# Kernel tuning notes

Hardware: AMD Instinct MI355X
Metric: run time of the kernel (lower is better)

Reference implementation:

```python
import jax, jax.numpy as jnp
import numpy as np

B = 8192
IN = 2048   # input_size
H = 2048    # hidden_size
D = IN + H  # combine feature dim = 4096


def setup_inputs() -> dict:
    key = jax.random.key(0)
    ks = jax.random.split(key, 11)
    s = 1.0 / np.sqrt(D)  # nn.Linear default init scale
    inp = {
        "input": jax.random.normal(ks[0], (B, D), jnp.float32),
        "hidden": jax.random.normal(ks[1], (B, D), jnp.float32),
        "cell": jax.random.normal(ks[2], (B, H), jnp.float32),
        "Wf": jax.random.uniform(ks[3], (D, H), jnp.float32, -s, s),
        "bf": jax.random.uniform(ks[4], (H,), jnp.float32, -s, s),
        "Wc": jax.random.uniform(ks[5], (D, H), jnp.float32, -s, s),
        "bc": jax.random.uniform(ks[6], (H,), jnp.float32, -s, s),
        "Wi": jax.random.uniform(ks[7], (D, H), jnp.float32, -s, s),
        "bi": jax.random.uniform(ks[8], (H,), jnp.float32, -s, s),
        "Wo": jax.random.uniform(ks[9], (D, H), jnp.float32, -s, s),
        "bo": jax.random.uniform(ks[10], (H,), jnp.float32, -s, s),
    }
    return inp


def reference(input, hidden, cell, Wf, bf, Wc, bc, Wi, bi, Wo, bo):
    combine = input + hidden  # [B, D] elementwise add (as in source, not concat)
    # Fuse the 4 gate GEMMs into one [D, 4H] GEMM for efficiency (same math).
    W = jnp.concatenate([Wf, Wc, Wi, Wo], axis=1)  # [D, 4H]
    b = jnp.concatenate([bf, bc, bi, bo])          # [4H]
    gates = combine @ W + b                        # [B, 4H]
    gf, gc, gi, go = jnp.split(gates, 4, axis=1)
    ft = jax.nn.sigmoid(gf)
    ct_ = jnp.tanh(gc)
    it = jax.nn.sigmoid(jax.nn.sigmoid(gi))  # double sigmoid, faithful to source
    cell_state = cell * ft + ct_ * it
    out = jax.nn.sigmoid(go)
    hidden_state = out * jnp.tanh(cell_state)
    return (out, hidden_state, cell_state)
```

## Files before the change

### kernel.cpp

```cpp
#include <hip/hip_runtime.h>
#include <hip/hip_bf16.h>

#define B_SZ 8192
#define D_SZ 4096
#define H_SZ 2048
#define N4H  8192
#define NT   (D_SZ / 64)

typedef __attribute__((ext_vector_type(8))) __bf16 bf16x8;
typedef __attribute__((ext_vector_type(4))) float f32x4;

#define GPTR(p) ((__attribute__((address_space(1))) void*)(p))
#define LPTR(p) ((__attribute__((address_space(3))) void*)(p))

__global__ void prep_k(const float* __restrict__ x, const float* __restrict__ h,
                       __hip_bfloat16* __restrict__ comb,
                       const float* __restrict__ Wf, const float* __restrict__ Wc,
                       const float* __restrict__ Wi, const float* __restrict__ Wo,
                       __hip_bfloat16* __restrict__ WT) {
    __shared__ float t[32][33];
    if (blockIdx.x < 2048) {
        const size_t n4 = (size_t)B_SZ * D_SZ / 4;
        const size_t stride = (size_t)2048 * 256;
        for (size_t i = (size_t)blockIdx.x * 256 + threadIdx.x; i < n4; i += stride) {
            f32x4 a = __builtin_nontemporal_load((const f32x4*)x + i);
            f32x4 b = __builtin_nontemporal_load((const f32x4*)h + i);
            short4 r;
            r.x = __builtin_bit_cast(short, __float2bfloat16(a.x + b.x));
            r.y = __builtin_bit_cast(short, __float2bfloat16(a.y + b.y));
            r.z = __builtin_bit_cast(short, __float2bfloat16(a.z + b.z));
            r.w = __builtin_bit_cast(short, __float2bfloat16(a.w + b.w));
            ((short4*)comb)[i] = r;
        }
    } else {
        const int b = blockIdx.x - 2048;
        const int k0 = (b & 127) * 32;
        const int n0 = (b >> 7) * 32;
        const float* W = (n0 < H_SZ) ? Wf : (n0 < 2 * H_SZ) ? Wc
                       : (n0 < 3 * H_SZ) ? Wi : Wo;
        const int g = n0 >> 11;
        const int nc = n0 & (H_SZ - 1);
        const int tx = threadIdx.x & 31, ty = threadIdx.x >> 5;
#pragma unroll
        for (int j = 0; j < 4; ++j)
            t[ty + j * 8][tx] = __builtin_nontemporal_load(
                W + (size_t)(k0 + ty + j * 8) * H_SZ + nc + tx);
        __syncthreads();
#pragma unroll
        for (int j = 0; j < 4; ++j) {
            const int h2 = nc + ty + j * 8;
            const int np = ((h2 >> 4) << 6) + (g << 4) + (h2 & 15);
            WT[(size_t)np * D_SZ + k0 + tx] = __float2bfloat16(t[tx][ty + j * 8]);
        }
    }
}


#define LDS_A0 0
#define LDS_A1 16384
#define LDS_BB0 32768
#define LDS_BB1 49152

#define BAR()                                    \
    do {                                         \
        asm volatile("" ::: "memory");           \
        __builtin_amdgcn_s_barrier();            \
        asm volatile("" ::: "memory");           \
    } while (0)

#define STAGE_A(h, kt)                                                                 \
    do {                                                                               \
        _Pragma("unroll") for (int c_ = 0; c_ < 4; ++c_) {                             \
            __builtin_amdgcn_global_load_lds(                                          \
                GPTR(pA + (size_t)((c_ >> 1) * 128 + (h) * 64 + (c_ & 1) * 32) * D_SZ  \
                         + (size_t)(kt) * 64),                                         \
                LPTR(smem + (h) * 16384 + c_ * 4096 + wave * 1024), 16, 0, 0);         \
        }                                                                              \
    } while (0)

#define STAGE_B(qn, kt, bb)                                                            \
    do {                                                                               \
        _Pragma("unroll") for (int c_ = 0; c_ < 2; ++c_) {                             \
            __builtin_amdgcn_global_load_lds(                                          \
                GPTR(pB + (size_t)((qn) * 32 + c_ * 64) * D_SZ + (size_t)(kt) * 64),   \
                LPTR(smem + (bb) + (qn) * 8192 + c_ * 4096 + wave * 1024), 16, 0, 0);  \
        }                                                                              \
    } while (0)

#define LDA(dst, RB)                                                                   \
    do {                                                                               \
        _Pragma("unroll") for (int mi = 0; mi < 4; ++mi) {                             \
            const int row_ = wr * 64 + mi * 16 + fr;                                   \
            dst[mi][0] = *(const bf16x8*)(smem + (RB) + row_ * 128 + sw0);             \
            dst[mi][1] = *(const bf16x8*)(smem + (RB) + row_ * 128 + sw1);             \
        }                                                                              \
    } while (0)

#define LDB(dst, BB, qn)                                                               \
    do {                                                                               \
        _Pragma("unroll") for (int nf = 0; nf < 2; ++nf) {                             \
            const int row_ = (qn) * 64 + wc * 32 + nf * 16 + fr;                       \
            dst[nf][0] = *(const bf16x8*)(smem + (BB) + row_ * 128 + sw0);             \
            dst[nf][1] = *(const bf16x8*)(smem + (BB) + row_ * 128 + sw1);             \
        }                                                                              \
    } while (0)

#define MFMA_Q(qm, qn, areg, breg)                                                     \
    do {                                                                               \
        _Pragma("unroll") for (int mi = 0; mi < 4; ++mi)                               \
        _Pragma("unroll") for (int nf = 0; nf < 2; ++nf)                               \
        _Pragma("unroll") for (int ks = 0; ks < 2; ++ks)                               \
            acc[(qm) * 4 + mi][(qn) * 2 + nf] =                                        \
                __builtin_amdgcn_mfma_f32_16x16x32_bf16(                               \
                    areg[mi][ks], breg[nf][ks],                                        \
                    acc[(qm) * 4 + mi][(qn) * 2 + nf], 0, 0, 0);                       \
    } while (0)

#define TILE(KT, CURB, OTHB)                                                           \
    {                                                                                  \
        const int kt_ = (KT) & 63;                                                     \
                             \
        STAGE_B(0, kt_, OTHB);                                                         \
        LDA(a, LDS_A0);                                                                \
        LDB(b0, CURB, 0);                                                              \
        __builtin_amdgcn_s_setprio(1);                                                 \
        MFMA_Q(0, 0, a, b0);                                                           \
        __builtin_amdgcn_s_setprio(0);                                                 \
        asm volatile("s_waitcnt vmcnt(6)" ::: "memory");                               \
        BAR();                                                                         \
                     \
        STAGE_A(0, kt_);                                                               \
        LDB(b1, CURB, 1);                                                              \
        __builtin_amdgcn_s_setprio(1);                                                 \
        MFMA_Q(0, 1, a, b1);                                                           \
        __builtin_amdgcn_s_setprio(0);                                                 \
        asm volatile("s_waitcnt vmcnt(6)" ::: "memory");                               \
        BAR();                                                                         \
                  \
        STAGE_B(1, kt_, OTHB);                                                         \
        LDA(a, LDS_A1);                                                                \
        __builtin_amdgcn_s_setprio(1);                                                 \
        MFMA_Q(1, 0, a, b0);                                                           \
        __builtin_amdgcn_s_setprio(0);                                                 \
        BAR();                                                                         \
                                  \
        STAGE_A(1, kt_);                                                               \
        __builtin_amdgcn_s_setprio(1);                                                 \
        MFMA_Q(1, 1, a, b1);                                                           \
        __builtin_amdgcn_s_setprio(0);                                                 \
        asm volatile("s_waitcnt vmcnt(6)" ::: "memory");                               \
        BAR();                                                                         \
    }

__device__ __forceinline__ float fsig(float x) { return 1.f / (1.f + __expf(-x)); }
__device__ __forceinline__ float ftanh(float x) {
    x = fminf(fmaxf(x, -15.f), 15.f);
    float e = __expf(2.f * x);
    return (e - 1.f) / (e + 1.f);
}

__global__ __launch_bounds__(256, 2) void gemm4_k(
    const __hip_bfloat16* __restrict__ A,
    const __hip_bfloat16* __restrict__ BT,
    const float* __restrict__ cell,
    const float* __restrict__ bfb, const float* __restrict__ bcb,
    const float* __restrict__ bib, const float* __restrict__ bob,
    float* __restrict__ out)
{
    extern __shared__ char smem[];

    const int tid  = threadIdx.x;
    const int wave = tid >> 6;
    const int lane = tid & 63;
    const int wr = wave >> 1;
    const int wc = wave & 1;
    const int fr = lane & 15;
    const int sw0 = (((lane >> 4) + 0) ^ (fr & 7)) << 4;
    const int sw1 = (((lane >> 4) + 4) ^ (fr & 7)) << 4;

    const int wg = (blockIdx.x & 7) * 256 + (blockIdx.x >> 3);
    const int ntile = wg & 63;
    const int m0 = (wg >> 6) * 256;
    const int n0 = ntile * 128;

    const int r0   = tid >> 3;
    const int col0 = ((tid & 7) ^ (r0 & 7)) << 3;
    const __hip_bfloat16* pA = A  + (size_t)(m0 + r0) * D_SZ + col0;
    const __hip_bfloat16* pB = BT + (size_t)(n0 + r0) * D_SZ + col0;

    f32x4 acc[8][4] = {};
    bf16x8 a[4][2], b0[2][2], b1[2][2];

    STAGE_B(0, 0, LDS_BB0);
    STAGE_A(0, 0);
    STAGE_B(1, 0, LDS_BB0);
    STAGE_A(1, 0);
    asm volatile("s_waitcnt vmcnt(6)" ::: "memory");
    BAR();

#pragma unroll 1
    for (int t = 0; t < NT; t += 2) {
        TILE(t + 1, LDS_BB0, LDS_BB1);
        TILE(t + 2, LDS_BB1, LDS_BB0);
    }

    {
        const int crow = (lane >> 4) * 4;
        const int ccol = lane & 15;
        const int hh = (ntile * 2 + wc) * 16 + ccol;
        const float bf_ = bfb[hh], bc_ = bcb[hh], bi_ = bib[hh], bo_ = bob[hh];
        const size_t BH = (size_t)B_SZ * H_SZ;
        float* hidp = out + BH;
        float* cstp = out + 2 * BH;
#pragma unroll
        for (int ai = 0; ai < 8; ++ai) {
#pragma unroll
            for (int j = 0; j < 4; ++j) {
                const size_t r = (size_t)(m0 + wr * 128 + ai * 16 + crow + j);
                const size_t idx = r * H_SZ + hh;
                const float gf = acc[ai][0][j] + bf_;
                const float gc = acc[ai][1][j] + bc_;
                const float gi = acc[ai][2][j] + bi_;
                const float go = acc[ai][3][j] + bo_;
                const float ft = fsig(gf);
                const float ct = ftanh(gc);
                const float it_ = fsig(fsig(gi));
                const float ot = fsig(go);
                const float cv = __builtin_nontemporal_load(cell + idx);
                const float cs = cv * ft + ct * it_;
                __builtin_nontemporal_store(ot, out + idx);
                __builtin_nontemporal_store(cs, cstp + idx);
                __builtin_nontemporal_store(ot * ftanh(cs), hidp + idx);
            }
        }
    }

    asm volatile("s_waitcnt vmcnt(0)" ::: "memory");
}

extern "C" void kernel_launch(void* const* d_in, const int* in_sizes, int n_in,
                              void* d_out, int out_size, void* d_ws, size_t ws_size,
                              hipStream_t stream) {
    const float* input  = (const float*)d_in[0];
    const float* hidden = (const float*)d_in[1];
    const float* cell   = (const float*)d_in[2];
    const float* Wf     = (const float*)d_in[3];
    const float* bfb    = (const float*)d_in[4];
    const float* Wc     = (const float*)d_in[5];
    const float* bcb    = (const float*)d_in[6];
    const float* Wi     = (const float*)d_in[7];
    const float* bib    = (const float*)d_in[8];
    const float* Wo     = (const float*)d_in[9];
    const float* bob    = (const float*)d_in[10];
    float* out = (float*)d_out;

    char* ws = (char*)d_ws;
    __hip_bfloat16* comb = (__hip_bfloat16*)ws;
    __hip_bfloat16* WT   = (__hip_bfloat16*)(ws + (size_t)B_SZ * D_SZ * 2);

    hipFuncSetAttribute(reinterpret_cast<const void*>(gemm4_k),
                        hipFuncAttributeMaxDynamicSharedMemorySize, 65536);

    prep_k<<<2048 + 32768, 256, 0, stream>>>(input, hidden, comb, Wf, Wc, Wi, Wo, WT);
    gemm4_k<<<2048, 256, 65536, stream>>>(comb, WT, cell, bfb, bcb, bib, bob, out);
}
```

Before: 598.5 us.

## Switch fused-gate GEMM to 32x32x16 MFMA with 128x256 tiles

Replaces the 16x16x32 bf16 MFMA tiling with 32x32x16 MFMAs. The block tile changes from 256x128 to 128x256 and the weight interleave goes from 16-column to 32-column gate groups, so each wave still holds all four gates for its columns. Staging, LDS layout and the epilogue row mapping are reworked to match, and dynamic LDS grows to 80KB. The aim is fewer MFMA issues and LDS reads per FLOP, at the cost of more LDS per block, which may hurt occupancy at two blocks per CU.

```diff
diff --git a/kernel.cpp b/kernel.cpp
--- a/kernel.cpp
+++ b/kernel.cpp
@@ -7,8 +7,9 @@
 #define N4H  8192
 #define NT   (D_SZ / 64)
 
-typedef __attribute__((ext_vector_type(8))) __bf16 bf16x8;
-typedef __attribute__((ext_vector_type(4))) float f32x4;
+typedef __attribute__((ext_vector_type(8)))  __bf16 bf16x8;
+typedef __attribute__((ext_vector_type(4)))  float  f32x4;
+typedef __attribute__((ext_vector_type(16))) float  f32x16;
 
 #define GPTR(p) ((__attribute__((address_space(1))) void*)(p))
 #define LPTR(p) ((__attribute__((address_space(3))) void*)(p))
@@ -49,16 +50,14 @@
 #pragma unroll
         for (int j = 0; j < 4; ++j) {
             const int h2 = nc + ty + j * 8;
-            const int np = ((h2 >> 4) << 6) + (g << 4) + (h2 & 15);
+            const int np = ((h2 >> 5) << 7) + (g << 5) + (h2 & 31);
             WT[(size_t)np * D_SZ + k0 + tx] = __float2bfloat16(t[tx][ty + j * 8]);
         }
     }
 }
 
 
-#define LDS_A0 0
-#define LDS_A1 16384
-#define LDS_BB0 32768
+#define LDS_BB0 16384
 #define LDS_BB1 49152
 
 #define BAR()                                    \
@@ -68,85 +67,78 @@
         asm volatile("" ::: "memory");           \
     } while (0)
 
-#define STAGE_A(h, kt)                                                                 \
+#define STAGE_A(mt, kt)                                                                \
+    do {                                                                               \
+        _Pragma("unroll") for (int c_ = 0; c_ < 2; ++c_) {                             \
+            const int ro_ = c_ * 64 + (mt) * 32;                                       \
+            __builtin_amdgcn_global_load_lds(                                          \
+                GPTR(pA + (size_t)ro_ * D_SZ + (size_t)(kt) * 64),                     \
+                LPTR(smem + (ro_ + wave * 8) * 128), 16, 0, 0);                        \
+        }                                                                              \
+    } while (0)
+
+#define STAGE_Bp(jp, kt, bb)                                                           \
     do {                                                                               \
         _Pragma("unroll") for (int c_ = 0; c_ < 4; ++c_) {                             \
+            const int ro_ = (c_ >> 1) * 128 + (jp) * 64 + (c_ & 1) * 32;               \
             __builtin_amdgcn_global_load_lds(                                          \
-                GPTR(pA + (size_t)((c_ >> 1) * 128 + (h) * 64 + (c_ & 1) * 32) * D_SZ  \
-                         + (size_t)(kt) * 64),                                         \
-                LPTR(smem + (h) * 16384 + c_ * 4096 + wave * 1024), 16, 0, 0);         \
+                GPTR(pB + (size_t)ro_ * D_SZ + (size_t)(kt) * 64),                     \
+                LPTR(smem + (bb) + (ro_ + wave * 8) * 128), 16, 0, 0);                 \
         }                                                                              \
     } while (0)
 
-#define STAGE_B(qn, kt, bb)                                                            \
-    do {                                                                               \
-        _Pragma("unroll") for (int c_ = 0; c_ < 2; ++c_) {                             \
-            __builtin_amdgcn_global_load_lds(                                          \
-                GPTR(pB + (size_t)((qn) * 32 + c_ * 64) * D_SZ + (size_t)(kt) * 64),   \
-                LPTR(smem + (bb) + (qn) * 8192 + c_ * 4096 + wave * 1024), 16, 0, 0);  \
-        }                                                                              \
-    } while (0)
-
-#define LDA(dst, RB)                                                                   \
-    do {                                                                               \
-        _Pragma("unroll") for (int mi = 0; mi < 4; ++mi) {                             \
-            const int row_ = wr * 64 + mi * 16 + fr;                                   \
-            dst[mi][0] = *(const bf16x8*)(smem + (RB) + row_ * 128 + sw0);             \
-            dst[mi][1] = *(const bf16x8*)(smem + (RB) + row_ * 128 + sw1);             \
-        }                                                                              \
-    } while (0)
-
-#define LDB(dst, BB, qn)                                                               \
-    do {                                                                               \
-        _Pragma("unroll") for (int nf = 0; nf < 2; ++nf) {                             \
-            const int row_ = (qn) * 64 + wc * 32 + nf * 16 + fr;                       \
-            dst[nf][0] = *(const bf16x8*)(smem + (BB) + row_ * 128 + sw0);             \
-            dst[nf][1] = *(const bf16x8*)(smem + (BB) + row_ * 128 + sw1);             \
-        }                                                                              \
-    } while (0)
-
-#define MFMA_Q(qm, qn, areg, breg)                                                     \
-    do {                                                                               \
-        _Pragma("unroll") for (int mi = 0; mi < 4; ++mi)                               \
-        _Pragma("unroll") for (int nf = 0; nf < 2; ++nf)                               \
-        _Pragma("unroll") for (int ks = 0; ks < 2; ++ks)                               \
-            acc[(qm) * 4 + mi][(qn) * 2 + nf] =                                        \
-                __builtin_amdgcn_mfma_f32_16x16x32_bf16(                               \
-                    areg[mi][ks], breg[nf][ks],                                        \
-                    acc[(qm) * 4 + mi][(qn) * 2 + nf], 0, 0, 0);                       \
+#define LDA(mt, AOFF)                                                                  \
+    do {                                                                               \
+        _Pragma("unroll") for (int k_ = 0; k_ < 4; ++k_)                               \
+            a[mt][k_] = *(const bf16x8*)(smem + (AOFF) + swk[k_]);                     \
+    } while (0)
+
+#define LDB2(jp, BUFB)                                                                 \
+    do {                                                                               \
+        _Pragma("unroll") for (int jj_ = 0; jj_ < 2; ++jj_)                            \
+        _Pragma("unroll") for (int k_ = 0; k_ < 4; ++k_)                               \
+            b[jj_][k_] = *(const bf16x8*)(smem + (BUFB) + boff[(jp) * 2 + jj_]         \
+                                          + swk[k_]);                                  \
+    } while (0)
+
+#define MFMA_P(mt, jp)                                                                 \
+    do {                                                                               \
+        _Pragma("unroll") for (int k_ = 0; k_ < 4; ++k_)                               \
+        _Pragma("unroll") for (int jj_ = 0; jj_ < 2; ++jj_)                            \
+            acc[mt][(jp) * 2 + jj_] = __builtin_amdgcn_mfma_f32_32x32x16_bf16(         \
+                a[mt][k_], b[jj_][k_], acc[mt][(jp) * 2 + jj_], 0, 0, 0);              \
     } while (0)
 
 #define TILE(KT, CURB, OTHB)                                                           \
     {                                                                                  \
         const int kt_ = (KT) & 63;                                                     \
-                             \
-        STAGE_B(0, kt_, OTHB);                                                         \
-        LDA(a, LDS_A0);                                                                \
-        LDB(b0, CURB, 0);                                                              \
-        __builtin_amdgcn_s_setprio(1);                                                 \
-        MFMA_Q(0, 0, a, b0);                                                           \
-        __builtin_amdgcn_s_setprio(0);                                                 \
-        asm volatile("s_waitcnt vmcnt(6)" ::: "memory");                               \
-        BAR();                                                                         \
-                     \
+                                                                              \
+        STAGE_Bp(0, kt_, OTHB);                                                        \
+        LDA(0, aoff0);                                                                 \
+        LDB2(0, CURB);                                                                 \
+        __builtin_amdgcn_s_setprio(1);                                                 \
+        MFMA_P(0, 0);                                                                  \
+        __builtin_amdgcn_s_setprio(0);                                                 \
+        asm volatile("s_waitcnt vmcnt(4)" ::: "memory");                               \
+        BAR();                                                                         \
+                                                                              \
         STAGE_A(0, kt_);                                                               \
-        LDB(b1, CURB, 1);                                                              \
-        __builtin_amdgcn_s_setprio(1);                                                 \
-        MFMA_Q(0, 1, a, b1);                                                           \
-        __builtin_amdgcn_s_setprio(0);                                                 \
-        asm volatile("s_waitcnt vmcnt(6)" ::: "memory");                               \
-        BAR();                                                                         \
-                  \
-        STAGE_B(1, kt_, OTHB);                                                         \
-        LDA(a, LDS_A1);                                                                \
-        __builtin_amdgcn_s_setprio(1);                                                 \
-        MFMA_Q(1, 0, a, b0);                                                           \
-        __builtin_amdgcn_s_setprio(0);                                                 \
-        BAR();                                                                         \
-                                  \
+        LDA(1, aoff1);                                                                 \
+        __builtin_amdgcn_s_setprio(1);                                                 \
+        MFMA_P(1, 0);                                                                  \
+        __builtin_amdgcn_s_setprio(0);                                                 \
+        BAR();                                                                         \
+                                                                              \
+        STAGE_Bp(1, kt_, OTHB);                                                        \
+        LDB2(1, CURB);                                                                 \
+        __builtin_amdgcn_s_setprio(1);                                                 \
+        MFMA_P(0, 1);                                                                  \
+        __builtin_amdgcn_s_setprio(0);                                                 \
+        BAR();                                                                         \
+                                                                              \
         STAGE_A(1, kt_);                                                               \
         __builtin_amdgcn_s_setprio(1);                                                 \
-        MFMA_Q(1, 1, a, b1);                                                           \
+        MFMA_P(1, 1);                                                                  \
         __builtin_amdgcn_s_setprio(0);                                                 \
         asm volatile("s_waitcnt vmcnt(6)" ::: "memory");                               \
         BAR();                                                                         \
@@ -159,7 +151,7 @@
     return (e - 1.f) / (e + 1.f);
 }
 
-__global__ __launch_bounds__(256, 2) void gemm4_k(
+__global__ __launch_bounds__(256, 2) void gemm32_k(
     const __hip_bfloat16* __restrict__ A,
     const __hip_bfloat16* __restrict__ BT,
     const float* __restrict__ cell,
@@ -174,26 +166,36 @@
     const int lane = tid & 63;
     const int wr = wave >> 1;
     const int wc = wave & 1;
-    const int fr = lane & 15;
-    const int sw0 = (((lane >> 4) + 0) ^ (fr & 7)) << 4;
-    const int sw1 = (((lane >> 4) + 4) ^ (fr & 7)) << 4;
+    const int l31 = lane & 31;
+    const int l7  = lane & 7;
+    const int khi = lane >> 5;
+
+    int swk[4];
+#pragma unroll
+    for (int k_ = 0; k_ < 4; ++k_) swk[k_] = ((k_ * 2 + khi) ^ l7) << 4;
+
+    const int aoff0 = (wr * 64 + 0 * 32 + l31) * 128;
+    const int aoff1 = (wr * 64 + 1 * 32 + l31) * 128;
+    int boff[4];
+#pragma unroll
+    for (int j_ = 0; j_ < 4; ++j_) boff[j_] = (wc * 128 + j_ * 32 + l31) * 128;
 
     const int wg = (blockIdx.x & 7) * 256 + (blockIdx.x >> 3);
-    const int ntile = wg & 63;
-    const int m0 = (wg >> 6) * 256;
-    const int n0 = ntile * 128;
-
-    const int r0   = tid >> 3;
-    const int col0 = ((tid & 7) ^ (r0 & 7)) << 3;
-    const __hip_bfloat16* pA = A  + (size_t)(m0 + r0) * D_SZ + col0;
-    const __hip_bfloat16* pB = BT + (size_t)(n0 + r0) * D_SZ + col0;
-
-    f32x4 acc[8][4] = {};
-    bf16x8 a[4][2], b0[2][2], b1[2][2];
-
-    STAGE_B(0, 0, LDS_BB0);
+    const int ntile = wg & 31;
+    const int m0 = (wg >> 5) * 128;
+    const int n0 = ntile * 256;
+
+    const int r8   = tid >> 3;
+    const int gcol = ((tid & 7) ^ (r8 & 7)) << 3;
+    const __hip_bfloat16* pA = A  + (size_t)(m0 + r8) * D_SZ + gcol;
+    const __hip_bfloat16* pB = BT + (size_t)(n0 + r8) * D_SZ + gcol;
+
+    f32x16 acc[2][4] = {};
+    bf16x8 a[2][4], b[2][4];
+
+    STAGE_Bp(0, 0, LDS_BB0);
     STAGE_A(0, 0);
-    STAGE_B(1, 0, LDS_BB0);
+    STAGE_Bp(1, 0, LDS_BB0);
     STAGE_A(1, 0);
     asm volatile("s_waitcnt vmcnt(6)" ::: "memory");
     BAR();
@@ -205,23 +207,23 @@
     }
 
     {
-        const int crow = (lane >> 4) * 4;
-        const int ccol = lane & 15;
-        const int hh = (ntile * 2 + wc) * 16 + ccol;
+        const int rbase = khi * 4;
+        const int hh = (ntile * 2 + wc) * 32 + l31;
         const float bf_ = bfb[hh], bc_ = bcb[hh], bi_ = bib[hh], bo_ = bob[hh];
         const size_t BH = (size_t)B_SZ * H_SZ;
         float* hidp = out + BH;
         float* cstp = out + 2 * BH;
 #pragma unroll
-        for (int ai = 0; ai < 8; ++ai) {
-#pragma unroll
-            for (int j = 0; j < 4; ++j) {
-                const size_t r = (size_t)(m0 + wr * 128 + ai * 16 + crow + j);
+        for (int mt = 0; mt < 2; ++mt) {
+#pragma unroll
+            for (int reg = 0; reg < 16; ++reg) {
+                const int rr = (reg & 3) + 8 * (reg >> 2) + rbase;
+                const size_t r = (size_t)(m0 + wr * 64 + mt * 32 + rr);
                 const size_t idx = r * H_SZ + hh;
-                const float gf = acc[ai][0][j] + bf_;
-                const float gc = acc[ai][1][j] + bc_;
-                const float gi = acc[ai][2][j] + bi_;
-                const float go = acc[ai][3][j] + bo_;
+                const float gf = acc[mt][0][reg] + bf_;
+                const float gc = acc[mt][1][reg] + bc_;
+                const float gi = acc[mt][2][reg] + bi_;
+                const float go = acc[mt][3][reg] + bo_;
                 const float ft = fsig(gf);
                 const float ct = ftanh(gc);
                 const float it_ = fsig(fsig(gi));
@@ -258,9 +260,9 @@
     __hip_bfloat16* comb = (__hip_bfloat16*)ws;
     __hip_bfloat16* WT   = (__hip_bfloat16*)(ws + (size_t)B_SZ * D_SZ * 2);
 
-    hipFuncSetAttribute(reinterpret_cast<const void*>(gemm4_k),
-                        hipFuncAttributeMaxDynamicSharedMemorySize, 65536);
+    hipFuncSetAttribute(reinterpret_cast<const void*>(gemm32_k),
+                        hipFuncAttributeMaxDynamicSharedMemorySize, 81920);
 
     prep_k<<<2048 + 32768, 256, 0, stream>>>(input, hidden, comb, Wf, Wc, Wi, Wo, WT);
-    gemm4_k<<<2048, 256, 65536, stream>>>(comb, WT, cell, bfb, bcb, bib, bob, out);
-}
+    gemm32_k<<<2048, 256, 81920, stream>>>(comb, WT, cell, bfb, bcb, bib, bob, out);
+}
```

Result: slower. 741.5 us (+23.9%).
